# Kernel tuning notes

Hardware: AMD Instinct MI355X
Metric: run time of the kernel (lower is better)

## Reference

```python
import jax, jax.numpy as jnp
import numpy as np

T, M = 8192, 64  # timesteps, number of correlated series


def setup_inputs() -> dict:
    key = jax.random.key(0)
    k_y, k_mu, k_sig = jax.random.split(key, 3)
    y = jax.random.normal(k_y, (T, M), dtype=jnp.float32)
    MU = (jax.random.normal(k_mu, (M,), dtype=jnp.float32) * 0.01)
    sigma0 = jax.random.uniform(k_sig, (M,), dtype=jnp.float32, minval=0.5, maxval=1.5)
    alpha0 = sigma0  # ctor initializes alpha0 = std(y,0) as well
    alpha = jnp.full((M,), 0.25, dtype=jnp.float32)
    beta = jnp.full((M,), 0.25, dtype=jnp.float32)
    # L0 = cholesky of a correlation matrix (ctor uses corrcoef(y.T))
    rng = np.random.default_rng(0)
    Z = rng.standard_normal((M, 4 * M)).astype(np.float64)
    C = Z @ Z.T
    d = np.sqrt(np.diag(C))
    C = C / np.outer(d, d)
    L0 = jnp.asarray(np.linalg.cholesky(C), dtype=jnp.float32)
    A = jnp.full((1,), 0.9, dtype=jnp.float32)
    B = jnp.full((1,), 0.05, dtype=jnp.float32)
    return dict(y=y, MU=MU, sigma0=sigma0, alpha0=alpha0, alpha=alpha,
                beta=beta, L0=L0, A=A, B=B)


def reference(y, MU, sigma0, alpha0, alpha, beta, L0, A, B):
    """DCC-GARCH conditional moments.
    Returns (mus [T,M], Sigmas [T,M,M]) — the parameters of the
    MultivariateNormalFullCovariance the TF model constructs.
    """
    n = y.shape[1]
    A0 = L0.T @ L0                  # unconditional correlation target (M,M)
    a0 = alpha0 ** 2                # (M,)

    def step(carry, y_t):
        u, sig, Q = carry           # u:(M,), sig:(M,), Q:(M,M)
        sig_t = jnp.sqrt(a0 + alpha * sig ** 2 + beta * u ** 2)
        ustd = u / sig
        Psi = jnp.outer(ustd, ustd)
        Q_t = A0 + A * (Q - A0) + B * (Psi - A0)
        dinv = 1.0 / jnp.sqrt(jnp.diagonal(Q_t))
        R_t = Q_t * jnp.outer(dinv, dinv)        # cov_to_corr
        Sigma_t = R_t * jnp.outer(sig_t, sig_t)  # D_t @ R_t @ D_t
        return (y_t - MU, sig_t, Q_t), Sigma_t

    u0 = jnp.zeros((n,), dtype=y.dtype)
    _, Sigmas = jax.lax.scan(step, (u0, sigma0, A0), y)
    mus = jnp.broadcast_to(MU, y.shape)
    return mus, Sigmas
```

## Files before the change

### kernel.cpp

```cpp
#include <hip/hip_runtime.h>
#include <hip/hip_bf16.h>
#include <stdint.h>

#define TT 8192
#define MM 64
#define CHUNK 32
#define WQ 96
#define WS 32
#define YROWS (CHUNK + WQ + WS)

__global__ __launch_bounds__(256, 2)
void dcc_kernel(const float* __restrict__ y, const float* __restrict__ MU,
                const float* __restrict__ sigma0, const float* __restrict__ alpha0,
                const float* __restrict__ alpha, const float* __restrict__ beta,
                const float* __restrict__ L0, const float* __restrict__ Ap,
                const float* __restrict__ Bp,
                float* __restrict__ out)
{
    __shared__ float lds_yu[YROWS][MM];
    __shared__ float lds_s[CHUNK][MM];

    const int tid  = threadIdx.x;
    const int c0   = blockIdx.x * CHUNK;
    const int cend = c0 + CHUNK;
    const int tq0  = (c0 > WQ) ? (c0 - WQ) : 0;
    const int ts0  = (tq0 > WS) ? (tq0 - WS) : 0;

    const float A = Ap[0], B = Bp[0];
    const float kappa = 1.0f - A - B;

    float* out_mu = out;
    float* out_sg = out + (size_t)TT * MM;

    {
        int o = tid * 8;
        int m = o & (MM - 1);
        float4 a = *(const float4*)(MU + m);
        float4 b = *(const float4*)(MU + m + 4);
        float* dst = out_mu + (size_t)c0 * MM + o;
        *(float4*)(dst)     = a;
        *(float4*)(dst + 4) = b;
    }

    {
        const float* ysrc = y + (size_t)ts0 * MM;
        const int nflt = (cend - ts0) * MM;
        for (int o = tid * 4; o < nflt; o += 256 * 4) {
            float4 v = *(const float4*)(ysrc + o);
            *(float4*)(&lds_yu[0][0] + o) = v;
        }
    }
    __syncthreads();

    if (tid < MM) {
        const int m = tid;
        const float mu  = MU[m];
        const float al  = alpha[m], be = beta[m];
        const float a0v = alpha0[m] * alpha0[m];
        float s2 = sigma0[m] * sigma0[m];
        float u_prev = (ts0 > 0) ? (y[(size_t)(ts0 - 1) * MM + m] - mu) : 0.0f;
        for (int t = ts0; t < cend; ++t) {
            float yt  = lds_yu[t - ts0][m];
            float s2n = fmaf(al, s2, fmaf(be, u_prev * u_prev, a0v));
            if (t >= tq0) lds_yu[t - tq0][m] = u_prev * rsqrtf(s2);
            if (t >= c0)  lds_s[t - c0][m]   = sqrtf(s2n);
            u_prev = yt - mu;
            s2 = s2n;
        }
    }

    const int j0 = (tid & 15) * 4;
    const int i0 = (tid >> 4) * 4;

    float acc[4][4], adr[4], adc[4];
    #pragma unroll
    for (int a = 0; a < 4; ++a) {
        adr[a] = 0.f; adc[a] = 0.f;
        #pragma unroll
        for (int b = 0; b < 4; ++b) acc[a][b] = 0.f;
    }
    #pragma unroll 4
    for (int k = 0; k < MM; ++k) {
        float4 Li = *(const float4*)(L0 + k * MM + i0);
        float4 Lj = *(const float4*)(L0 + k * MM + j0);
        float li[4] = {Li.x, Li.y, Li.z, Li.w};
        float lj[4] = {Lj.x, Lj.y, Lj.z, Lj.w};
        #pragma unroll
        for (int a = 0; a < 4; ++a) {
            #pragma unroll
            for (int b = 0; b < 4; ++b)
                acc[a][b] = fmaf(li[a], lj[b], acc[a][b]);
            adr[a] = fmaf(li[a], li[a], adr[a]);
            adc[a] = fmaf(lj[a], lj[a], adc[a]);
        }
    }
    __syncthreads();

    float q[4][4], Cm[4][4], qdr[4], qdc[4], Cdr[4], Cdc[4];
    #pragma unroll
    for (int a = 0; a < 4; ++a) {
        qdr[a] = adr[a]; Cdr[a] = kappa * adr[a];
        qdc[a] = adc[a]; Cdc[a] = kappa * adc[a];
        #pragma unroll
        for (int b = 0; b < 4; ++b) {
            q[a][b]  = acc[a][b];
            Cm[a][b] = kappa * acc[a][b];
        }
    }

    for (int t = tq0; t < cend; ++t) {
        const int r = t - tq0;
        float4 U_i = *(const float4*)(&lds_yu[r][i0]);
        float4 U_j = *(const float4*)(&lds_yu[r][j0]);
        float ui[4] = {U_i.x, U_i.y, U_i.z, U_i.w};
        float uj[4] = {U_j.x, U_j.y, U_j.z, U_j.w};
        #pragma unroll
        for (int a = 0; a < 4; ++a) {
            float bui = B * ui[a];
            #pragma unroll
            for (int b = 0; b < 4; ++b)
                q[a][b] = fmaf(A, q[a][b], fmaf(bui, uj[b], Cm[a][b]));
            qdr[a] = fmaf(A, qdr[a], fmaf(bui, ui[a], Cdr[a]));
            float buj = B * uj[a];
            qdc[a] = fmaf(A, qdc[a], fmaf(buj, uj[a], Cdc[a]));
        }
        if (t >= c0) {
            float4 S_i = *(const float4*)(&lds_s[t - c0][i0]);
            float4 S_j = *(const float4*)(&lds_s[t - c0][j0]);
            float ri[4] = { S_i.x * rsqrtf(qdr[0]), S_i.y * rsqrtf(qdr[1]),
                            S_i.z * rsqrtf(qdr[2]), S_i.w * rsqrtf(qdr[3]) };
            float rj[4] = { S_j.x * rsqrtf(qdc[0]), S_j.y * rsqrtf(qdc[1]),
                            S_j.z * rsqrtf(qdc[2]), S_j.w * rsqrtf(qdc[3]) };
            float* o = out_sg + ((size_t)t << 12) + (i0 << 6) + j0;
            #pragma unroll
            for (int a = 0; a < 4; ++a) {
                float f = ri[a];
                float4 w;
                w.x = q[a][0] * f * rj[0];
                w.y = q[a][1] * f * rj[1];
                w.z = q[a][2] * f * rj[2];
                w.w = q[a][3] * f * rj[3];
                *(float4*)(o + a * MM) = w;
            }
        }
    }
}

extern "C" void kernel_launch(void* const* d_in, const int* in_sizes, int n_in,
                              void* d_out, int out_size, void* d_ws, size_t ws_size,
                              hipStream_t stream) {
    (void)in_sizes; (void)n_in; (void)out_size; (void)d_ws; (void)ws_size;
    const float* y      = (const float*)d_in[0];
    const float* MU     = (const float*)d_in[1];
    const float* sigma0 = (const float*)d_in[2];
    const float* alpha0 = (const float*)d_in[3];
    const float* alpha  = (const float*)d_in[4];
    const float* beta   = (const float*)d_in[5];
    const float* L0     = (const float*)d_in[6];
    const float* A      = (const float*)d_in[7];
    const float* B      = (const float*)d_in[8];
    dcc_kernel<<<dim3(TT / CHUNK), dim3(256), 0, stream>>>(
        y, MU, sigma0, alpha0, alpha, beta, L0, A, B, (float*)d_out);
}
```

Before: 182.5 us.

## Split each chunk's correlation matrix rows across two blocks and shorten warm-up windows

Each time chunk is now handled by two blocks, each computing half of the 64 rows of the Q/Sigma matrix (2x4 tiles per thread instead of 4x4), doubling the grid to 512 blocks. The Q and sigma warm-up windows are cut from 96/32 to 64/16 steps, reducing the redundant recurrence work per block. The scalar sigma recurrence and the L0 product are now duplicated across both halves. The shorter warm-up relies on A^t decay and may slightly change accuracy.

```diff
diff --git a/kernel.cpp b/kernel.cpp
--- a/kernel.cpp
+++ b/kernel.cpp
@@ -5,9 +5,10 @@
 #define TT 8192
 #define MM 64
 #define CHUNK 32
-#define WQ 96
-#define WS 32
+#define WQ 64
+#define WS 16
 #define YROWS (CHUNK + WQ + WS)
+#define NSPLIT 2
 
 __global__ __launch_bounds__(256, 2)
 void dcc_kernel(const float* __restrict__ y, const float* __restrict__ MU,
@@ -21,7 +22,9 @@
     __shared__ float lds_s[CHUNK][MM];
 
     const int tid  = threadIdx.x;
-    const int c0   = blockIdx.x * CHUNK;
+    const int chnk = blockIdx.x >> 1;
+    const int h    = blockIdx.x & 1;
+    const int c0   = chnk * CHUNK;
     const int cend = c0 + CHUNK;
     const int tq0  = (c0 > WQ) ? (c0 - WQ) : 0;
     const int ts0  = (tq0 > WS) ? (tq0 - WS) : 0;
@@ -32,7 +35,7 @@
     float* out_mu = out;
     float* out_sg = out + (size_t)TT * MM;
 
-    {
+    if (h == 0) {
         int o = tid * 8;
         int m = o & (MM - 1);
         float4 a = *(const float4*)(MU + m);
@@ -70,70 +73,78 @@
     }
 
     const int j0 = (tid & 15) * 4;
-    const int i0 = (tid >> 4) * 4;
+    const int i0 = h * 32 + (tid >> 4) * 2;
 
-    float acc[4][4], adr[4], adc[4];
+    float acc[2][4], adr[2], adc[4];
     #pragma unroll
-    for (int a = 0; a < 4; ++a) {
-        adr[a] = 0.f; adc[a] = 0.f;
+    for (int a = 0; a < 2; ++a) { adr[a] = 0.f; }
+    #pragma unroll
+    for (int b = 0; b < 4; ++b) { adc[b] = 0.f; }
+    #pragma unroll
+    for (int a = 0; a < 2; ++a)
         #pragma unroll
         for (int b = 0; b < 4; ++b) acc[a][b] = 0.f;
-    }
+
     #pragma unroll 4
     for (int k = 0; k < MM; ++k) {
-        float4 Li = *(const float4*)(L0 + k * MM + i0);
+        float2 Li = *(const float2*)(L0 + k * MM + i0);
         float4 Lj = *(const float4*)(L0 + k * MM + j0);
-        float li[4] = {Li.x, Li.y, Li.z, Li.w};
+        float li[2] = {Li.x, Li.y};
         float lj[4] = {Lj.x, Lj.y, Lj.z, Lj.w};
         #pragma unroll
-        for (int a = 0; a < 4; ++a) {
+        for (int a = 0; a < 2; ++a) {
             #pragma unroll
             for (int b = 0; b < 4; ++b)
                 acc[a][b] = fmaf(li[a], lj[b], acc[a][b]);
             adr[a] = fmaf(li[a], li[a], adr[a]);
-            adc[a] = fmaf(lj[a], lj[a], adc[a]);
         }
+        #pragma unroll
+        for (int b = 0; b < 4; ++b)
+            adc[b] = fmaf(lj[b], lj[b], adc[b]);
     }
     __syncthreads();
 
-    float q[4][4], Cm[4][4], qdr[4], qdc[4], Cdr[4], Cdc[4];
+    float q[2][4], Cm[2][4], qdr[2], qdc[4], Cdr[2], Cdc[4];
     #pragma unroll
-    for (int a = 0; a < 4; ++a) {
-        qdr[a] = adr[a]; Cdr[a] = kappa * adr[a];
-        qdc[a] = adc[a]; Cdc[a] = kappa * adc[a];
+    for (int a = 0; a < 2; ++a) { qdr[a] = adr[a]; Cdr[a] = kappa * adr[a]; }
+    #pragma unroll
+    for (int b = 0; b < 4; ++b) { qdc[b] = adc[b]; Cdc[b] = kappa * adc[b]; }
+    #pragma unroll
+    for (int a = 0; a < 2; ++a)
         #pragma unroll
         for (int b = 0; b < 4; ++b) {
             q[a][b]  = acc[a][b];
             Cm[a][b] = kappa * acc[a][b];
         }
-    }
 
     for (int t = tq0; t < cend; ++t) {
         const int r = t - tq0;
-        float4 U_i = *(const float4*)(&lds_yu[r][i0]);
+        float2 U_i = *(const float2*)(&lds_yu[r][i0]);
         float4 U_j = *(const float4*)(&lds_yu[r][j0]);
-        float ui[4] = {U_i.x, U_i.y, U_i.z, U_i.w};
+        float ui[2] = {U_i.x, U_i.y};
         float uj[4] = {U_j.x, U_j.y, U_j.z, U_j.w};
         #pragma unroll
-        for (int a = 0; a < 4; ++a) {
+        for (int a = 0; a < 2; ++a) {
             float bui = B * ui[a];
             #pragma unroll
             for (int b = 0; b < 4; ++b)
                 q[a][b] = fmaf(A, q[a][b], fmaf(bui, uj[b], Cm[a][b]));
             qdr[a] = fmaf(A, qdr[a], fmaf(bui, ui[a], Cdr[a]));
-            float buj = B * uj[a];
-            qdc[a] = fmaf(A, qdc[a], fmaf(buj, uj[a], Cdc[a]));
+        }
+        #pragma unroll
+        for (int b = 0; b < 4; ++b) {
+            float buj = B * uj[b];
+            qdc[b] = fmaf(A, qdc[b], fmaf(buj, uj[b], Cdc[b]));
         }
         if (t >= c0) {
-            float4 S_i = *(const float4*)(&lds_s[t - c0][i0]);
+            float2 S_i = *(const float2*)(&lds_s[t - c0][i0]);
             float4 S_j = *(const float4*)(&lds_s[t - c0][j0]);
-            float ri[4] = { S_i.x * rsqrtf(qdr[0]), S_i.y * rsqrtf(qdr[1]),
-                            S_i.z * rsqrtf(qdr[2]), S_i.w * rsqrtf(qdr[3]) };
+            float ri[2] = { S_i.x * rsqrtf(qdr[0]), S_i.y * rsqrtf(qdr[1]) };
             float rj[4] = { S_j.x * rsqrtf(qdc[0]), S_j.y * rsqrtf(qdc[1]),
                             S_j.z * rsqrtf(qdc[2]), S_j.w * rsqrtf(qdc[3]) };
             float* o = out_sg + ((size_t)t << 12) + (i0 << 6) + j0;
             #pragma unroll
-            for (int a = 0; a < 4; ++a) {
+            for (int a = 0; a < 2; ++a) {
                 float f = ri[a];
                 float4 w;
                 w.x = q[a][0] * f * rj[0];
@@ -159,6 +170,6 @@
     const float* L0     = (const float*)d_in[6];
     const float* A      = (const float*)d_in[7];
     const float* B      = (const float*)d_in[8];
-    dcc_kernel<<<dim3(TT / CHUNK), dim3(256), 0, stream>>>(
+    dcc_kernel<<<dim3((TT / CHUNK) * NSPLIT), dim3(256), 0, stream>>>(
         y, MU, sigma0, alpha0, alpha, beta, L0, A, B, (float*)d_out);
 }
```

After: 171.0 us. 6.3% less time.
